# Optimization experiments

Measured on AMD Instinct MI355X. Metric: run time of the kernel, lower is better.

## Reference

```python
import jax, jax.numpy as jnp
import numpy as np

H, KVH, D, HID = 32, 8, 128, 4096
ROPE_LEN, THETA = 8192, 10000.0
MASK_OUT, MIN_REMAIN = 0.9, 128


def _rope_tables(dtype):
    inv_freq = 1.0 / (THETA ** (jnp.arange(0, D, 2, dtype=jnp.float32) / D))
    freqs = jnp.arange(ROPE_LEN, dtype=jnp.float32)[:, None] * inv_freq[None, :]
    emb = jnp.concatenate([freqs, freqs], axis=-1)  # [8192, 128]
    return jnp.cos(emb).astype(dtype), jnp.sin(emb).astype(dtype)


def _rotate_half(x):
    x1, x2 = x[..., : D // 2], x[..., D // 2:]
    return jnp.concatenate([-x2, x1], axis=-1)


def _apply_rope(x, pos, cos, sin):
    c, s = cos[pos][None, None], sin[pos][None, None]  # [1,1,L,D]
    return x * c + _rotate_half(x) * s


def setup_inputs() -> dict:
    key = jax.random.key(0)
    ks = jax.random.split(key, 11)
    S = 4096
    f = jnp.float32
    return {
        "hidden_states": jax.random.normal(ks[0], (1, 1, HID), f),
        "key_cache": jax.random.normal(ks[1], (1, H, S, D), f),
        "val_cache": jax.random.normal(ks[2], (1, H, S, D), f),
        "Wq": jax.random.normal(ks[3], (HID, HID), f) * 0.02,
        "Wk": jax.random.normal(ks[4], (HID, KVH * D), f) * 0.02,
        "Wv": jax.random.normal(ks[5], (HID, KVH * D), f) * 0.02,
        "Wo": jax.random.normal(ks[6], (HID, HID), f) * 0.02,
        "hash_proj1": jax.random.normal(ks[7], (1, H, D, D), f) * 0.001,
        "hash_bias1": jnp.zeros((1, H, 1, D), f),
        "hash_proj2": jax.random.normal(ks[8], (1, H, D, D), f) * 0.001,
        "hash_bias2": jnp.zeros((1, H, 1, D), f),
    }


def reference(hidden_states, key_cache, val_cache, Wq, Wk, Wv, Wo,
              hash_proj1, hash_bias1, hash_proj2, hash_bias2):
    B, Q, _ = hidden_states.shape  # B=1, Q=1 (decode step)
    G = H // KVH
    dtype = hidden_states.dtype

    # projections -> [B, heads, Q, D]
    ques = (hidden_states @ Wq).reshape(B, Q, H, D).transpose(0, 2, 1, 3)
    k_new = (hidden_states @ Wk).reshape(B, Q, KVH, D).transpose(0, 2, 1, 3)
    v_new = (hidden_states @ Wv).reshape(B, Q, KVH, D).transpose(0, 2, 1, 3)
    k_new = jnp.repeat(k_new, G, axis=1)  # repeat_kv
    v_new = jnp.repeat(v_new, G, axis=1)

    keys = jnp.concatenate([key_cache, k_new], axis=2)  # [1,H,K,D]
    vals = jnp.concatenate([val_cache, v_new], axis=2)
    K = keys.shape[2]

    cos, sin = _rope_tables(dtype)
    q_pos = K - Q + jnp.arange(Q)
    k_pos = jnp.arange(K)
    q_r = _apply_rope(ques, q_pos, cos, sin)
    k_r = _apply_rope(keys, k_pos, cos, sin)

    # per-head hash MLP: silu layer with residue, then linear layer with residue
    def hash_fn(x):
        h = jax.nn.silu(jnp.einsum('bhld,bhde->bhle', x, hash_proj1) + hash_bias1) + x
        h = (jnp.einsum('bhld,bhde->bhle', h, hash_proj2) + hash_bias2) + h
        return h

    q_hash = jnp.sign(hash_fn(q_r))
    k_hash = jnp.sign(hash_fn(k_r))
    draft_score = jnp.einsum('bhqd,bhkd->bhqk', q_hash, k_hash)  # LSH similarity

    num_remain = max(min(K, MIN_REMAIN), K - int(K * MASK_OUT))
    _, idx = jax.lax.top_k(draft_score, num_remain)  # [B,H,Q,num_remain]

    neg = jnp.finfo(dtype).min
    mask = jnp.full((B, H, Q, K), neg, dtype=dtype)
    bi = jnp.arange(B)[:, None, None, None]
    hi = jnp.arange(H)[None, :, None, None]
    qi = jnp.arange(Q)[None, None, :, None]
    mask = mask.at[bi, hi, qi, idx].set(0.0)

    scores = jnp.einsum('bhqd,bhkd->bhqk', q_r, k_r) / np.sqrt(D) + mask
    attn = jax.nn.softmax(scores, axis=-1)
    out = jnp.einsum('bhqk,bhkd->bhqd', attn, vals)
    out = out.transpose(0, 2, 1, 3).reshape(B, Q, HID) @ Wo
    return out
```

## Files before the change

### kernel.cpp

```cpp
#include <hip/hip_runtime.h>
#include <math.h>

#define NH 32
#define NKVH 8
#define HD 128

typedef _Float16 half8 __attribute__((ext_vector_type(8)));
typedef float f32x4 __attribute__((ext_vector_type(4)));

#define OFF_QPROJ 0
#define OFF_KNEW  4096
#define OFF_VNEW  5120
#define OFF_QR    6144
#define OFF_QHASH 10240
#define OFF_TAB   10368

__global__ void init_kernel(const float* __restrict__ hp1, const float* __restrict__ hp2,
                            float* __restrict__ ws, float* __restrict__ out,
                            int K, int nInit) {
    const int tid = threadIdx.x;
    if ((int)blockIdx.x < nInit) {
        int idx = blockIdx.x * 256 + tid;
        if (idx < K * 64) {
            int pos = idx >> 6, d = idx & 63;
            double inv = exp(-((double)d / 64.0) * log(10000.0));
            double ang = (double)pos * inv;
            double s, c;
            sincos(ang, &s, &c);
            ws[OFF_TAB + idx]                  = (float)c;
            ws[OFF_TAB + (size_t)K * 64 + idx] = (float)s;
        }
        if (idx < 6144) ws[OFF_QPROJ + idx] = 0.f;
        if (idx < 4096) out[idx] = 0.f;
        size_t off_attn = OFF_TAB + 2 * (size_t)K * 64 + 2 * (size_t)NH * K;
        if (idx < 4096) ws[off_attn + idx] = 0.f;
    } else {
        int id = blockIdx.x - nInit;
        int h2 = id >> 3;
        int tg = (id & 7) * 256 + tid;
        const int lane = tg & 63, nt = (tg >> 6) & 7, ks = tg >> 9;
        const int kbase = ks * 32 + ((tg >> 4) & 3) * 8;
        const int n = nt * 16 + (tg & 15);
        const float* P = ((h2 & 1) ? hp2 : hp1) + (size_t)(h2 >> 1) * 16384;
        half8 v;
#pragma unroll
        for (int j = 0; j < 8; ++j) v[j] = (_Float16)P[(size_t)(kbase + j) * 128 + n];
        size_t off_pt = OFF_TAB + 2 * (size_t)K * 64 + 2 * (size_t)NH * K + 4096 + 2 * (size_t)NH * 512;
        ((half8*)(ws + off_pt))[(size_t)h2 * 2048 + tg] = v;
    }
}

__global__ __launch_bounds__(256) void qkv_gemv(const float* __restrict__ hidden,
        const float* __restrict__ Wq, const float* __restrict__ Wk,
        const float* __restrict__ Wv, float* __restrict__ ws) {
    __shared__ float hs[64];
    const int tid = threadIdx.x;
    const int col = (blockIdx.x * 256 + tid) * 4;
    const int i0  = blockIdx.y * 64;
    if (tid < 64) hs[tid] = hidden[i0 + tid];
    __syncthreads();
    const float* W; int ld, wcol;
    if (col < 4096)      { W = Wq; ld = 4096; wcol = col; }
    else if (col < 5120) { W = Wk; ld = 1024; wcol = col - 4096; }
    else                 { W = Wv; ld = 1024; wcol = col - 5120; }
    const float* p = W + (size_t)i0 * ld + wcol;
    float4 a0 = {0.f,0.f,0.f,0.f}, a1 = {0.f,0.f,0.f,0.f};
#pragma unroll 4
    for (int ii = 0; ii < 64; ii += 2) {
        float4 w0 = *(const float4*)p;
        float4 w1 = *(const float4*)(p + ld);
        float h0 = hs[ii], h1 = hs[ii + 1];
        a0.x = fmaf(h0, w0.x, a0.x); a0.y = fmaf(h0, w0.y, a0.y);
        a0.z = fmaf(h0, w0.z, a0.z); a0.w = fmaf(h0, w0.w, a0.w);
        a1.x = fmaf(h1, w1.x, a1.x); a1.y = fmaf(h1, w1.y, a1.y);
        a1.z = fmaf(h1, w1.z, a1.z); a1.w = fmaf(h1, w1.w, a1.w);
        p += 2 * (size_t)ld;
    }
    atomicAdd(&ws[OFF_QPROJ + col + 0], a0.x + a1.x);
    atomicAdd(&ws[OFF_QPROJ + col + 1], a0.y + a1.y);
    atomicAdd(&ws[OFF_QPROJ + col + 2], a0.z + a1.z);
    atomicAdd(&ws[OFF_QPROJ + col + 3], a0.w + a1.w);
}

__global__ __launch_bounds__(128) void qhash_kernel(const float* __restrict__ hp1,
        const float* __restrict__ hb1, const float* __restrict__ hp2,
        const float* __restrict__ hb2, float* __restrict__ ws, int S) {
    const int h = blockIdx.x, d = threadIdx.x;
    const int K = S + 1;
    __shared__ float X[128], H1[128];
    float q  = ws[OFF_QPROJ + h * 128 + d];
    float qp = ws[OFF_QPROJ + h * 128 + (d ^ 64)];
    const float* cosT = ws + OFF_TAB;
    const float* sinT = cosT + (size_t)K * 64;
    float cs = cosT[(size_t)S * 64 + (d & 63)];
    float sn = sinT[(size_t)S * 64 + (d & 63)];
    float r = (d < 64) ? -qp : qp;
    float qr = q * cs + r * sn;
    X[d] = qr;
    ws[OFF_QR + h * 128 + d] = qr;
    __syncthreads();
    const float* P1 = hp1 + (size_t)h * 16384;
    float t = hb1[h * 128 + d];
    for (int i = 0; i < 128; ++i) t = fmaf(X[i], P1[i * 128 + d], t);
    float u = t / (1.f + expf(-t)) + X[d];
    H1[d] = u;
    __syncthreads();
    const float* P2 = hp2 + (size_t)h * 16384;
    float t2 = hb2[h * 128 + d] + u;
    for (int i = 0; i < 128; ++i) t2 = fmaf(H1[i], P2[i * 128 + d], t2);
    unsigned long long bal = __ballot(t2 > 0.f);
    if ((d & 63) == 0)
        ((unsigned long long*)(ws + OFF_QHASH))[h * 2 + (d >> 6)] = bal;
}

__global__ __launch_bounds__(256, 3) void key_kernel(const float* __restrict__ key_cache,
        const float* __restrict__ hb1, const float* __restrict__ hb2,
        float* __restrict__ ws, int S) {
    const int K  = S + 1;
    const int h  = blockIdx.y;
    const int k0 = blockIdx.x * 64;
    const int tid = threadIdx.x;
    const int wv = tid >> 6, lane = tid & 63;
    const int m = lane & 15, quad = lane >> 4;

    __shared__ float    XF[64 * 132];
    __shared__ _Float16 XH[64 * 136];

    const float* cosT = ws + OFF_TAB;
    const float* sinT = cosT + (size_t)K * 64;
    float* scores = ws + OFF_TAB + 2 * (size_t)K * 64;
    int*   draft  = (int*)(scores + (size_t)NH * K);
    size_t off_pt = OFF_TAB + 2 * (size_t)K * 64 + 2 * (size_t)NH * K + 4096 + 2 * (size_t)NH * 512;
    const half8* PT1 = (const half8*)((const _Float16*)(ws + off_pt) + (size_t)(h * 2) * 16384);
    const half8* PT2 = PT1 + 2048;

    const int key = tid >> 2, qq = tid & 3, d0 = qq * 16;
    const int kg = k0 + key;
    float lo[16], hi[16];
    if (kg < K) {
        const float* row = (kg < S) ? key_cache + ((size_t)h * S + kg) * 128
                                    : ws + OFF_KNEW + (h >> 2) * 128;
#pragma unroll
        for (int i4 = 0; i4 < 4; ++i4) {
            float4 xa = *(const float4*)(row + d0 + i4 * 4);
            float4 xb = *(const float4*)(row + 64 + d0 + i4 * 4);
            float4 cc = *(const float4*)(cosT + (size_t)kg * 64 + d0 + i4 * 4);
            float4 ss = *(const float4*)(sinT + (size_t)kg * 64 + d0 + i4 * 4);
            lo[i4*4+0] = xa.x * cc.x - xb.x * ss.x;  hi[i4*4+0] = xb.x * cc.x + xa.x * ss.x;
            lo[i4*4+1] = xa.y * cc.y - xb.y * ss.y;  hi[i4*4+1] = xb.y * cc.y + xa.y * ss.y;
            lo[i4*4+2] = xa.z * cc.z - xb.z * ss.z;  hi[i4*4+2] = xb.z * cc.z + xa.z * ss.z;
            lo[i4*4+3] = xa.w * cc.w - xb.w * ss.w;  hi[i4*4+3] = xb.w * cc.w + xa.w * ss.w;
        }
    } else {
#pragma unroll
        for (int i = 0; i < 16; ++i) { lo[i] = 0.f; hi[i] = 0.f; }
    }
#pragma unroll
    for (int i4 = 0; i4 < 4; ++i4) {
        float4 l4 = {lo[i4*4], lo[i4*4+1], lo[i4*4+2], lo[i4*4+3]};
        float4 h4 = {hi[i4*4], hi[i4*4+1], hi[i4*4+2], hi[i4*4+3]};
        *(float4*)&XF[key * 132 + d0 + i4 * 4]      = l4;
        *(float4*)&XF[key * 132 + 64 + d0 + i4 * 4] = h4;
    }
    {
        half8 hl0, hl1, hh0, hh1;
#pragma unroll
        for (int i = 0; i < 8; ++i) {
            hl0[i] = (_Float16)lo[i];     hl1[i] = (_Float16)lo[8 + i];
            hh0[i] = (_Float16)hi[i];     hh1[i] = (_Float16)hi[8 + i];
        }
        *(half8*)&XH[key * 136 + d0]          = hl0;
        *(half8*)&XH[key * 136 + d0 + 8]      = hl1;
        *(half8*)&XH[key * 136 + 64 + d0]     = hh0;
        *(half8*)&XH[key * 136 + 64 + d0 + 8] = hh1;
    }

    {
        const float* qr = ws + OFF_QR + h * 128;
        float part = 0.f;
#pragma unroll
        for (int i4 = 0; i4 < 4; ++i4) {
            float4 qa = *(const float4*)(qr + d0 + i4 * 4);
            float4 qb = *(const float4*)(qr + 64 + d0 + i4 * 4);
            part = fmaf(qa.x, lo[i4*4+0], fmaf(qb.x, hi[i4*4+0], part));
            part = fmaf(qa.y, lo[i4*4+1], fmaf(qb.y, hi[i4*4+1], part));
            part = fmaf(qa.z, lo[i4*4+2], fmaf(qb.z, hi[i4*4+2], part));
            part = fmaf(qa.w, lo[i4*4+3], fmaf(qb.w, hi[i4*4+3], part));
        }
        part += __shfl_xor(part, 1);
        part += __shfl_xor(part, 2);
        if (qq == 0 && kg < K) scores[(size_t)h * K + kg] = part * 0.08838834764831845f;
    }

    float b1v[8], b2v[8];
#pragma unroll
    for (int nt = 0; nt < 8; ++nt) {
        b1v[nt] = hb1[h * 128 + nt * 16 + m];
        b2v[nt] = hb2[h * 128 + nt * 16 + m];
    }
    unsigned short qh16[8];
    {
        uint4 q4 = *(const uint4*)((const unsigned*)(ws + OFF_QHASH) + h * 4);
        unsigned qa[4] = {q4.x, q4.y, q4.z, q4.w};
#pragma unroll
        for (int nt = 0; nt < 8; ++nt)
            qh16[nt] = (unsigned short)((qa[nt >> 1] >> ((nt & 1) * 16)) & 0xFFFFu);
    }

    f32x4 acc[8];

#define GEMM_MFMA(PT)                                                              \
    {                                                                              \
        _Pragma("unroll") for (int nt = 0; nt < 8; ++nt)                           \
            acc[nt] = (f32x4){0.f, 0.f, 0.f, 0.f};                                 \
        _Pragma("unroll") for (int c = 0; c < 4; ++c) {                            \
            half8 afrag = *(const half8*)&XH[(wv * 16 + m) * 136 + c * 32 + quad * 8]; \
            _Pragma("unroll") for (int nt = 0; nt < 8; ++nt) {                     \
                half8 bfrag = (PT)[c * 512 + nt * 64 + lane];                      \
                acc[nt] = __builtin_amdgcn_mfma_f32_16x16x32_f16(afrag, bfrag, acc[nt], 0, 0, 0); \
            }                                                                      \
        }                                                                          \
    }

    GEMM_MFMA(PT1)
#pragma unroll
    for (int nt = 0; nt < 8; ++nt) {
        const int n = nt * 16 + m;
#pragma unroll
        for (int r = 0; r < 4; ++r) {
            const int kk = wv * 16 + quad * 4 + r;
            float t = acc[nt][r] + b1v[nt];
            float x = XF[kk * 132 + n];
            float h1v = t / (1.f + expf(-t)) + x;
            XF[kk * 132 + n] = h1v;
            XH[kk * 136 + n] = (_Float16)h1v;
        }
    }

    GEMM_MFMA(PT2)
    {
        int ham[4] = {0, 0, 0, 0};
#pragma unroll
        for (int nt = 0; nt < 8; ++nt) {
            const int n = nt * 16 + m;
#pragma unroll
            for (int r = 0; r < 4; ++r) {
                const int kk = wv * 16 + quad * 4 + r;
                float t2 = acc[nt][r] + b2v[nt] + XF[kk * 132 + n];
                unsigned long long bal = __ballot(t2 > 0.f);
                unsigned bits = (unsigned)(bal >> (quad * 16)) & 0xFFFFu;
                ham[r] += __popc(bits ^ (unsigned)qh16[nt]);
            }
        }
        if (m == 0) {
#pragma unroll
            for (int r = 0; r < 4; ++r) {
                int kgd = k0 + wv * 16 + quad * 4 + r;
                if (kgd < K) draft[(size_t)h * K + kgd] = 128 - 2 * ham[r];
            }
        }
    }
#undef GEMM_MFMA
}

__global__ __launch_bounds__(256) void select_kernel(float* __restrict__ ws, int S, int nrem) {
    const int K = S + 1;
    const int h = blockIdx.x;
    const int tid = threadIdx.x;
    __shared__ int hist[129];
    __shared__ int sel_idx[512];
    __shared__ float red[256];
    __shared__ int wtot[4];
    __shared__ int sh_tval, sh_r, sh_cnt, sh_run;

    float* scoresB = ws + OFF_TAB + 2 * (size_t)K * 64;
    const int* draft = (const int*)(scoresB + (size_t)NH * K) + (size_t)h * K;
    const float* sc = scoresB + (size_t)h * K;
    float* attn = scoresB + 2 * (size_t)NH * K;
    int*   selidx_g = (int*)(attn + 4096) + h * 512;
    float* selw_g   = (attn + 4096 + NH * 512) + h * 512;

    for (int i = tid; i < 129; i += 256) hist[i] = 0;
    if (tid == 0) { sh_cnt = 0; sh_run = 0; }
    __syncthreads();
    for (int k = tid; k < K; k += 256) atomicAdd(&hist[(draft[k] + 128) >> 1], 1);
    __syncthreads();
    if (tid == 0) {
        int cum = 0, tb = 0, r = nrem;
        for (int b = 128; b >= 0; --b) {
            int c = hist[b];
            if (cum + c >= nrem) { tb = b; r = nrem - cum; break; }
            cum += c;
        }
        sh_tval = tb * 2 - 128; sh_r = r;
    }
    __syncthreads();
    const int tval = sh_tval, r = sh_r;
    const int lane = tid & 63, wave = tid >> 6;
    for (int base = 0; base < K; base += 256) {
        int k = base + tid;
        bool valid = (k < K);
        int dv = valid ? draft[k] : -1000;
        bool eq = valid && (dv == tval);
        bool gt = valid && (dv > tval);
        unsigned long long bal = __ballot(eq);
        if (lane == 0) wtot[wave] = __popcll(bal);
        __syncthreads();
        int woff = 0;
        for (int w = 0; w < wave; ++w) woff += wtot[w];
        int rank = sh_run + woff + __popcll(bal & ((1ull << lane) - 1ull));
        bool sel = gt || (eq && (rank < r));
        if (sel) sel_idx[atomicAdd(&sh_cnt, 1)] = k;
        __syncthreads();
        if (tid == 0) sh_run += wtot[0] + wtot[1] + wtot[2] + wtot[3];
        __syncthreads();
    }
    float mmax = -3.402823466e38f;
    for (int li = tid; li < nrem; li += 256) mmax = fmaxf(mmax, sc[sel_idx[li]]);
    red[tid] = mmax; __syncthreads();
    for (int s2 = 128; s2 > 0; s2 >>= 1) {
        if (tid < s2) red[tid] = fmaxf(red[tid], red[tid + s2]);
        __syncthreads();
    }
    mmax = red[0]; __syncthreads();
    float z = 0.f;
    for (int li = tid; li < nrem; li += 256) z += expf(sc[sel_idx[li]] - mmax);
    red[tid] = z; __syncthreads();
    for (int s2 = 128; s2 > 0; s2 >>= 1) {
        if (tid < s2) red[tid] += red[tid + s2];
        __syncthreads();
    }
    float Z = red[0]; __syncthreads();
    for (int li = tid; li < nrem; li += 256) {
        int idx = sel_idx[li];
        selidx_g[li] = idx;
        selw_g[li] = expf(sc[idx] - mmax) / Z;
    }
}

__global__ __launch_bounds__(256) void gather_kernel(const float* __restrict__ val_cache,
        float* __restrict__ ws, int S, int nrem) {
    const int K = S + 1;
    const int h = blockIdx.x, g = blockIdx.y;
    const int tid = threadIdx.x;
    const int wave = tid >> 6, lane = tid & 63;
    const int stream = g * 4 + wave;
    float* scoresB = ws + OFF_TAB + 2 * (size_t)K * 64;
    float* attn = scoresB + 2 * (size_t)NH * K;
    const int*   selidx_g = (const int*)(attn + 4096) + h * 512;
    const float* selw_g   = (attn + 4096 + NH * 512) + h * 512;
    float ax = 0.f, ay = 0.f;
    for (int li = stream; li < nrem; li += 64) {
        int idx = selidx_g[li];
        float w = selw_g[li];
        const float* vr = (idx < S) ? val_cache + ((size_t)h * S + idx) * 128
                                    : ws + OFF_VNEW + (h >> 2) * 128;
        float2 v = ((const float2*)vr)[lane];
        ax = fmaf(w, v.x, ax);
        ay = fmaf(w, v.y, ay);
    }
    atomicAdd(&attn[h * 128 + lane * 2 + 0], ax);
    atomicAdd(&attn[h * 128 + lane * 2 + 1], ay);
}

__global__ __launch_bounds__(256) void out_gemv(const float* __restrict__ Wo,
        const float* __restrict__ ws, float* __restrict__ out, int K) {
    __shared__ float hs[64];
    const int tid = threadIdx.x;
    const int col = (blockIdx.x * 256 + tid) * 4;
    const int i0  = blockIdx.y * 64;
    const float* ao = ws + OFF_TAB + 2 * (size_t)K * 64 + 2 * (size_t)NH * K;
    if (tid < 64) hs[tid] = ao[i0 + tid];
    __syncthreads();
    const float* p = Wo + (size_t)i0 * 4096 + col;
    float4 a0 = {0.f,0.f,0.f,0.f}, a1 = {0.f,0.f,0.f,0.f};
#pragma unroll 4
    for (int ii = 0; ii < 64; ii += 2) {
        float4 w0 = *(const float4*)p;
        float4 w1 = *(const float4*)(p + 4096);
        float h0 = hs[ii], h1 = hs[ii + 1];
        a0.x = fmaf(h0, w0.x, a0.x); a0.y = fmaf(h0, w0.y, a0.y);
        a0.z = fmaf(h0, w0.z, a0.z); a0.w = fmaf(h0, w0.w, a0.w);
        a1.x = fmaf(h1, w1.x, a1.x); a1.y = fmaf(h1, w1.y, a1.y);
        a1.z = fmaf(h1, w1.z, a1.z); a1.w = fmaf(h1, w1.w, a1.w);
        p += 8192;
    }
    atomicAdd(&out[col + 0], a0.x + a1.x);
    atomicAdd(&out[col + 1], a0.y + a1.y);
    atomicAdd(&out[col + 2], a0.z + a1.z);
    atomicAdd(&out[col + 3], a0.w + a1.w);
}

extern "C" void kernel_launch(void* const* d_in, const int* in_sizes, int n_in,
                              void* d_out, int out_size, void* d_ws, size_t ws_size,
                              hipStream_t stream) {
    const float* hidden = (const float*)d_in[0];
    const float* key_cache = (const float*)d_in[1];
    const float* val_cache = (const float*)d_in[2];
    const float* Wq = (const float*)d_in[3];
    const float* Wk = (const float*)d_in[4];
    const float* Wv = (const float*)d_in[5];
    const float* Wo = (const float*)d_in[6];
    const float* hp1 = (const float*)d_in[7];
    const float* hb1 = (const float*)d_in[8];
    const float* hp2 = (const float*)d_in[9];
    const float* hb2 = (const float*)d_in[10];
    float* out = (float*)d_out;
    float* ws  = (float*)d_ws;

    const int S = in_sizes[1] / (NH * HD);
    const int K = S + 1;
    int mn = (K < 128) ? K : 128;
    int nrem = K - (int)((double)K * 0.9);
    if (nrem < mn) nrem = mn;

    const int nInit = (K * 64 + 255) / 256;
    init_kernel<<<nInit + 512, 256, 0, stream>>>(hp1, hp2, ws, out, K, nInit);
    qkv_gemv<<<dim3(6, 64), 256, 0, stream>>>(hidden, Wq, Wk, Wv, ws);
    qhash_kernel<<<NH, 128, 0, stream>>>(hp1, hb1, hp2, hb2, ws, S);
    key_kernel<<<dim3((K + 63) / 64, NH), 256, 0, stream>>>(key_cache, hb1, hb2, ws, S);
    select_kernel<<<NH, 256, 0, stream>>>(ws, S, nrem);
    gather_kernel<<<dim3(NH, 16), 256, 0, stream>>>(val_cache, ws, S, nrem);
    out_gemv<<<dim3(4, 64), 256, 0, stream>>>(Wo, ws, out, K);
}
```

Before: 346.1 us.

## Drop fp16 LDS tile in key kernel, raise occupancy, and widen GEMV and gather grids

The key kernel now loads each key row in MFMA A-fragment layout, so the A operands are built directly in registers and the separate fp16 LDS tile is gone. The second GEMM converts from the fp32 LDS buffer instead. Launch bounds rise from 3 to 4 blocks per CU. The qkv and output GEMVs split the reduction dimension into twice as many blocks, and the gather kernel uses twice as many streams, to increase parallelism for the memory-bound phases at the cost of more atomics.

After: 359.6 us. 1.04x slower.

```diff
diff --git a/kernel.cpp b/kernel.cpp
--- a/kernel.cpp
+++ b/kernel.cpp
@@ -53,11 +53,11 @@
 __global__ __launch_bounds__(256) void qkv_gemv(const float* __restrict__ hidden,
         const float* __restrict__ Wq, const float* __restrict__ Wk,
         const float* __restrict__ Wv, float* __restrict__ ws) {
-    __shared__ float hs[64];
+    __shared__ float hs[32];
     const int tid = threadIdx.x;
     const int col = (blockIdx.x * 256 + tid) * 4;
-    const int i0  = blockIdx.y * 64;
-    if (tid < 64) hs[tid] = hidden[i0 + tid];
+    const int i0  = blockIdx.y * 32;
+    if (tid < 32) hs[tid] = hidden[i0 + tid];
     __syncthreads();
     const float* W; int ld, wcol;
     if (col < 4096)      { W = Wq; ld = 4096; wcol = col; }
@@ -66,7 +66,7 @@
     const float* p = W + (size_t)i0 * ld + wcol;
     float4 a0 = {0.f,0.f,0.f,0.f}, a1 = {0.f,0.f,0.f,0.f};
 #pragma unroll 4
-    for (int ii = 0; ii < 64; ii += 2) {
+    for (int ii = 0; ii < 32; ii += 2) {
         float4 w0 = *(const float4*)p;
         float4 w1 = *(const float4*)(p + ld);
         float h0 = hs[ii], h1 = hs[ii + 1];
@@ -113,7 +113,7 @@
         ((unsigned long long*)(ws + OFF_QHASH))[h * 2 + (d >> 6)] = bal;
 }
 
-__global__ __launch_bounds__(256, 3) void key_kernel(const float* __restrict__ key_cache,
+__global__ __launch_bounds__(256, 4) void key_kernel(const float* __restrict__ key_cache,
         const float* __restrict__ hb1, const float* __restrict__ hb2,
         float* __restrict__ ws, int S) {
     const int K  = S + 1;
@@ -123,8 +123,7 @@
     const int wv = tid >> 6, lane = tid & 63;
     const int m = lane & 15, quad = lane >> 4;
 
-    __shared__ float    XF[64 * 132];
-    __shared__ _Float16 XH[64 * 136];
+    __shared__ float XF[64 * 132];
 
     const float* cosT = ws + OFF_TAB;
     const float* sinT = cosT + (size_t)K * 64;
@@ -134,119 +133,127 @@
     const half8* PT1 = (const half8*)((const _Float16*)(ws + off_pt) + (size_t)(h * 2) * 16384);
     const half8* PT2 = PT1 + 2048;
 
-    const int key = tid >> 2, qq = tid & 3, d0 = qq * 16;
-    const int kg = k0 + key;
-    float lo[16], hi[16];
+    const int row = wv * 16 + m;
+    const int kg  = k0 + row;
+    const int cbase = quad * 8;
+    float xr[4][8];
     if (kg < K) {
-        const float* row = (kg < S) ? key_cache + ((size_t)h * S + kg) * 128
-                                    : ws + OFF_KNEW + (h >> 2) * 128;
-#pragma unroll
-        for (int i4 = 0; i4 < 4; ++i4) {
-            float4 xa = *(const float4*)(row + d0 + i4 * 4);
-            float4 xb = *(const float4*)(row + 64 + d0 + i4 * 4);
-            float4 cc = *(const float4*)(cosT + (size_t)kg * 64 + d0 + i4 * 4);
-            float4 ss = *(const float4*)(sinT + (size_t)kg * 64 + d0 + i4 * 4);
-            lo[i4*4+0] = xa.x * cc.x - xb.x * ss.x;  hi[i4*4+0] = xb.x * cc.x + xa.x * ss.x;
-            lo[i4*4+1] = xa.y * cc.y - xb.y * ss.y;  hi[i4*4+1] = xb.y * cc.y + xa.y * ss.y;
-            lo[i4*4+2] = xa.z * cc.z - xb.z * ss.z;  hi[i4*4+2] = xb.z * cc.z + xa.z * ss.z;
-            lo[i4*4+3] = xa.w * cc.w - xb.w * ss.w;  hi[i4*4+3] = xb.w * cc.w + xa.w * ss.w;
-        }
+        const float* krow = (kg < S) ? key_cache + ((size_t)h * S + kg) * 128
+                                     : ws + OFF_KNEW + (h >> 2) * 128;
+        float xv[4][8];
+#pragma unroll
+        for (int c = 0; c < 4; ++c) {
+            *(float4*)&xv[c][0] = *(const float4*)(krow + c * 32 + cbase);
+            *(float4*)&xv[c][4] = *(const float4*)(krow + c * 32 + cbase + 4);
+        }
+        float cc[2][8], ss[2][8];
+#pragma unroll
+        for (int c = 0; c < 2; ++c) {
+            *(float4*)&cc[c][0] = *(const float4*)(cosT + (size_t)kg * 64 + c * 32 + cbase);
+            *(float4*)&cc[c][4] = *(const float4*)(cosT + (size_t)kg * 64 + c * 32 + cbase + 4);
+            *(float4*)&ss[c][0] = *(const float4*)(sinT + (size_t)kg * 64 + c * 32 + cbase);
+            *(float4*)&ss[c][4] = *(const float4*)(sinT + (size_t)kg * 64 + c * 32 + cbase + 4);
+        }
+#pragma unroll
+        for (int c = 0; c < 2; ++c)
+#pragma unroll
+            for (int j = 0; j < 8; ++j) {
+                xr[c][j]     = xv[c][j]     * cc[c][j] - xv[c + 2][j] * ss[c][j];
+                xr[c + 2][j] = xv[c + 2][j] * cc[c][j] + xv[c][j]     * ss[c][j];
+            }
     } else {
 #pragma unroll
-        for (int i = 0; i < 16; ++i) { lo[i] = 0.f; hi[i] = 0.f; }
-    }
-#pragma unroll
-    for (int i4 = 0; i4 < 4; ++i4) {
-        float4 l4 = {lo[i4*4], lo[i4*4+1], lo[i4*4+2], lo[i4*4+3]};
-        float4 h4 = {hi[i4*4], hi[i4*4+1], hi[i4*4+2], hi[i4*4+3]};
-        *(float4*)&XF[key * 132 + d0 + i4 * 4]      = l4;
-        *(float4*)&XF[key * 132 + 64 + d0 + i4 * 4] = h4;
-    }
-    {
-        half8 hl0, hl1, hh0, hh1;
-#pragma unroll
-        for (int i = 0; i < 8; ++i) {
-            hl0[i] = (_Float16)lo[i];     hl1[i] = (_Float16)lo[8 + i];
-            hh0[i] = (_Float16)hi[i];     hh1[i] = (_Float16)hi[8 + i];
-        }
-        *(half8*)&XH[key * 136 + d0]          = hl0;
-        *(half8*)&XH[key * 136 + d0 + 8]      = hl1;
-        *(half8*)&XH[key * 136 + 64 + d0]     = hh0;
-        *(half8*)&XH[key * 136 + 64 + d0 + 8] = hh1;
+        for (int c = 0; c < 4; ++c)
+#pragma unroll
+            for (int j = 0; j < 8; ++j) xr[c][j] = 0.f;
+    }
+
+#pragma unroll
+    for (int c = 0; c < 4; ++c) {
+        *(float4*)&XF[row * 132 + c * 32 + cbase]     = *(float4*)&xr[c][0];
+        *(float4*)&XF[row * 132 + c * 32 + cbase + 4] = *(float4*)&xr[c][4];
     }
 
     {
         const float* qr = ws + OFF_QR + h * 128;
         float part = 0.f;
 #pragma unroll
-        for (int i4 = 0; i4 < 4; ++i4) {
-            float4 qa = *(const float4*)(qr + d0 + i4 * 4);
-            float4 qb = *(const float4*)(qr + 64 + d0 + i4 * 4);
-            part = fmaf(qa.x, lo[i4*4+0], fmaf(qb.x, hi[i4*4+0], part));
-            part = fmaf(qa.y, lo[i4*4+1], fmaf(qb.y, hi[i4*4+1], part));
-            part = fmaf(qa.z, lo[i4*4+2], fmaf(qb.z, hi[i4*4+2], part));
-            part = fmaf(qa.w, lo[i4*4+3], fmaf(qb.w, hi[i4*4+3], part));
-        }
-        part += __shfl_xor(part, 1);
-        part += __shfl_xor(part, 2);
-        if (qq == 0 && kg < K) scores[(size_t)h * K + kg] = part * 0.08838834764831845f;
-    }
-
-    float b1v[8], b2v[8];
-#pragma unroll
-    for (int nt = 0; nt < 8; ++nt) {
-        b1v[nt] = hb1[h * 128 + nt * 16 + m];
-        b2v[nt] = hb2[h * 128 + nt * 16 + m];
-    }
-    unsigned short qh16[8];
-    {
-        uint4 q4 = *(const uint4*)((const unsigned*)(ws + OFF_QHASH) + h * 4);
-        unsigned qa[4] = {q4.x, q4.y, q4.z, q4.w};
+        for (int c = 0; c < 4; ++c) {
+            float4 qa = *(const float4*)(qr + c * 32 + cbase);
+            float4 qb = *(const float4*)(qr + c * 32 + cbase + 4);
+            part = fmaf(qa.x, xr[c][0], part); part = fmaf(qa.y, xr[c][1], part);
+            part = fmaf(qa.z, xr[c][2], part); part = fmaf(qa.w, xr[c][3], part);
+            part = fmaf(qb.x, xr[c][4], part); part = fmaf(qb.y, xr[c][5], part);
+            part = fmaf(qb.z, xr[c][6], part); part = fmaf(qb.w, xr[c][7], part);
+        }
+        part += __shfl_xor(part, 16);
+        part += __shfl_xor(part, 32);
+        if (quad == 0 && kg < K) scores[(size_t)h * K + kg] = part * 0.08838834764831845f;
+    }
+
+    half8 af[4];
+#pragma unroll
+    for (int c = 0; c < 4; ++c)
+#pragma unroll
+        for (int j = 0; j < 8; ++j) af[c][j] = (_Float16)xr[c][j];
+
+    f32x4 acc[8];
+
+#pragma unroll
+    for (int nt = 0; nt < 8; ++nt) acc[nt] = (f32x4){0.f, 0.f, 0.f, 0.f};
+#pragma unroll
+    for (int c = 0; c < 4; ++c)
 #pragma unroll
         for (int nt = 0; nt < 8; ++nt)
-            qh16[nt] = (unsigned short)((qa[nt >> 1] >> ((nt & 1) * 16)) & 0xFFFFu);
-    }
-
-    f32x4 acc[8];
-
-#define GEMM_MFMA(PT)                                                              \
-    {                                                                              \
-        _Pragma("unroll") for (int nt = 0; nt < 8; ++nt)                           \
-            acc[nt] = (f32x4){0.f, 0.f, 0.f, 0.f};                                 \
-        _Pragma("unroll") for (int c = 0; c < 4; ++c) {                            \
-            half8 afrag = *(const half8*)&XH[(wv * 16 + m) * 136 + c * 32 + quad * 8]; \
-            _Pragma("unroll") for (int nt = 0; nt < 8; ++nt) {                     \
-                half8 bfrag = (PT)[c * 512 + nt * 64 + lane];                      \
-                acc[nt] = __builtin_amdgcn_mfma_f32_16x16x32_f16(afrag, bfrag, acc[nt], 0, 0, 0); \
-            }                                                                      \
-        }                                                                          \
-    }
-
-    GEMM_MFMA(PT1)
+            acc[nt] = __builtin_amdgcn_mfma_f32_16x16x32_f16(af[c], PT1[c * 512 + nt * 64 + lane], acc[nt], 0, 0, 0);
+
 #pragma unroll
     for (int nt = 0; nt < 8; ++nt) {
         const int n = nt * 16 + m;
+        float b1v = hb1[h * 128 + n];
 #pragma unroll
         for (int r = 0; r < 4; ++r) {
             const int kk = wv * 16 + quad * 4 + r;
-            float t = acc[nt][r] + b1v[nt];
+            float t = acc[nt][r] + b1v;
             float x = XF[kk * 132 + n];
             float h1v = t / (1.f + expf(-t)) + x;
             XF[kk * 132 + n] = h1v;
-            XH[kk * 136 + n] = (_Float16)h1v;
-        }
-    }
-
-    GEMM_MFMA(PT2)
+        }
+    }
+
+#pragma unroll
+    for (int nt = 0; nt < 8; ++nt) acc[nt] = (f32x4){0.f, 0.f, 0.f, 0.f};
+#pragma unroll
+    for (int c = 0; c < 4; ++c) {
+        float4 f0 = *(const float4*)&XF[row * 132 + c * 32 + cbase];
+        float4 f1 = *(const float4*)&XF[row * 132 + c * 32 + cbase + 4];
+        half8 a2;
+        a2[0] = (_Float16)f0.x; a2[1] = (_Float16)f0.y;
+        a2[2] = (_Float16)f0.z; a2[3] = (_Float16)f0.w;
+        a2[4] = (_Float16)f1.x; a2[5] = (_Float16)f1.y;
+        a2[6] = (_Float16)f1.z; a2[7] = (_Float16)f1.w;
+#pragma unroll
+        for (int nt = 0; nt < 8; ++nt)
+            acc[nt] = __builtin_amdgcn_mfma_f32_16x16x32_f16(a2, PT2[c * 512 + nt * 64 + lane], acc[nt], 0, 0, 0);
+    }
+
     {
+        unsigned short qh16[8];
+        uint4 q4 = *(const uint4*)((const unsigned*)(ws + OFF_QHASH) + h * 4);
+        unsigned qa[4] = {q4.x, q4.y, q4.z, q4.w};
+#pragma unroll
+        for (int nt = 0; nt < 8; ++nt)
+            qh16[nt] = (unsigned short)((qa[nt >> 1] >> ((nt & 1) * 16)) & 0xFFFFu);
+
         int ham[4] = {0, 0, 0, 0};
 #pragma unroll
         for (int nt = 0; nt < 8; ++nt) {
             const int n = nt * 16 + m;
+            float b2v = hb2[h * 128 + n];
 #pragma unroll
             for (int r = 0; r < 4; ++r) {
                 const int kk = wv * 16 + quad * 4 + r;
-                float t2 = acc[nt][r] + b2v[nt] + XF[kk * 132 + n];
+                float t2 = acc[nt][r] + b2v + XF[kk * 132 + n];
                 unsigned long long bal = __ballot(t2 > 0.f);
                 unsigned bits = (unsigned)(bal >> (quad * 16)) & 0xFFFFu;
                 ham[r] += __popc(bits ^ (unsigned)qh16[nt]);
@@ -260,7 +267,6 @@
             }
         }
     }
-#undef GEMM_MFMA
 }
 
 __global__ __launch_bounds__(256) void select_kernel(float* __restrict__ ws, int S, int nrem) {
@@ -350,7 +356,7 @@
     const int*   selidx_g = (const int*)(attn + 4096) + h * 512;
     const float* selw_g   = (attn + 4096 + NH * 512) + h * 512;
     float ax = 0.f, ay = 0.f;
-    for (int li = stream; li < nrem; li += 64) {
+    for (int li = stream; li < nrem; li += 128) {
         int idx = selidx_g[li];
         float w = selw_g[li];
         const float* vr = (idx < S) ? val_cache + ((size_t)h * S + idx) * 128
@@ -365,17 +371,17 @@
 
 __global__ __launch_bounds__(256) void out_gemv(const float* __restrict__ Wo,
         const float* __restrict__ ws, float* __restrict__ out, int K) {
-    __shared__ float hs[64];
+    __shared__ float hs[32];
     const int tid = threadIdx.x;
     const int col = (blockIdx.x * 256 + tid) * 4;
-    const int i0  = blockIdx.y * 64;
+    const int i0  = blockIdx.y * 32;
     const float* ao = ws + OFF_TAB + 2 * (size_t)K * 64 + 2 * (size_t)NH * K;
-    if (tid < 64) hs[tid] = ao[i0 + tid];
+    if (tid < 32) hs[tid] = ao[i0 + tid];
     __syncthreads();
     const float* p = Wo + (size_t)i0 * 4096 + col;
     float4 a0 = {0.f,0.f,0.f,0.f}, a1 = {0.f,0.f,0.f,0.f};
 #pragma unroll 4
-    for (int ii = 0; ii < 64; ii += 2) {
+    for (int ii = 0; ii < 32; ii += 2) {
         float4 w0 = *(const float4*)p;
         float4 w1 = *(const float4*)(p + 4096);
         float h0 = hs[ii], h1 = hs[ii + 1];
@@ -416,10 +422,10 @@
 
     const int nInit = (K * 64 + 255) / 256;
     init_kernel<<<nInit + 512, 256, 0, stream>>>(hp1, hp2, ws, out, K, nInit);
-    qkv_gemv<<<dim3(6, 64), 256, 0, stream>>>(hidden, Wq, Wk, Wv, ws);
+    qkv_gemv<<<dim3(6, 128), 256, 0, stream>>>(hidden, Wq, Wk, Wv, ws);
     qhash_kernel<<<NH, 128, 0, stream>>>(hp1, hb1, hp2, hb2, ws, S);
     key_kernel<<<dim3((K + 63) / 64, NH), 256, 0, stream>>>(key_cache, hb1, hb2, ws, S);
     select_kernel<<<NH, 256, 0, stream>>>(ws, S, nrem);
-    gather_kernel<<<dim3(NH, 16), 256, 0, stream>>>(val_cache, ws, S, nrem);
-    out_gemv<<<dim3(4, 64), 256, 0, stream>>>(Wo, ws, out, K);
-}
+    gather_kernel<<<dim3(NH, 32), 256, 0, stream>>>(val_cache, ws, S, nrem);
+    out_gemv<<<dim3(4, 128), 256, 0, stream>>>(Wo, ws, out, K);
+}
```
